# Performance work log

Measured on AMD Instinct MI355X. Metric: run time of the kernel, lower is better.

## Reference

```python
import jax, jax.numpy as jnp
import numpy as np

# Binary (sign) weight linear: y = x @ sign(W)^T + b

def _binarize(w):
    # sign with sign(0) mapped to +1, as in typical BinaryLinear impls
    return jnp.where(w >= 0, 1.0, -1.0).astype(w.dtype)

def setup_inputs() -> dict:
    key = jax.random.key(0)
    ks = jax.random.split(key, 7)
    B = 65536
    x = jax.random.normal(ks[0], (B, 28, 28), dtype=jnp.float32)
    W1 = jax.random.normal(ks[1], (1000, 784), dtype=jnp.float32) * 0.05
    b1 = jax.random.normal(ks[2], (1000,), dtype=jnp.float32) * 0.01
    W2 = jax.random.normal(ks[3], (500, 1000), dtype=jnp.float32) * 0.05
    b2 = jax.random.normal(ks[4], (500,), dtype=jnp.float32) * 0.01
    W3 = jax.random.normal(ks[5], (10, 500), dtype=jnp.float32) * 0.05
    b3 = jax.random.normal(ks[6], (10,), dtype=jnp.float32) * 0.01
    return {"x": x, "W1": W1, "b1": b1, "W2": W2, "b2": b2, "W3": W3, "b3": b3}

def reference(x, W1, b1, W2, b2, W3, b3):
    h = x.reshape(x.shape[0], -1)                      # [B, 784]
    h = jnp.maximum(h @ _binarize(W1).T + b1, 0.0)     # [B, 1000]
    h = jnp.maximum(h @ _binarize(W2).T + b2, 0.0)     # [B, 500]
    return h @ _binarize(W3).T + b3                    # [B, 10]
```

## Files before the change

kernel.cpp:

```cpp
#include <hip/hip_runtime.h>
#include <stdint.h>


typedef __attribute__((ext_vector_type(8))) short bf16x8;
typedef __attribute__((ext_vector_type(4))) float f32x4;

typedef const __attribute__((address_space(1))) unsigned int* as1_u32p;
typedef __attribute__((address_space(3))) unsigned int* as3_u32p;

__device__ __forceinline__ void glds16(const void* g, void* l) {
  __builtin_amdgcn_global_load_lds((as1_u32p)g, (as3_u32p)l, 16, 0, 0);
}

__device__ __forceinline__ unsigned short f2bf(float f) {
  union { float f; unsigned u; } c;
  c.f = f;
  unsigned u = c.u;
  u += 0x7FFFu + ((u >> 16) & 1u);
  return (unsigned short)(u >> 16);
}

__global__ void binarize_kernel(const float* __restrict__ src, int Ns, int Ks,
                                short* __restrict__ dst, int Np, int Kp) {
  int idx = blockIdx.x * 256 + threadIdx.x;
  if (idx >= Np * Kp) return;
  int n = idx / Kp;
  int k = idx - n * Kp;
  short v = 0;
  if (n < Ns && k < Ks)
    v = (src[n * Ks + k] >= 0.0f) ? (short)0x3F80 : (short)0xBF80;
  dst[idx] = v;
}

__global__ void convert_x_kernel(const float* __restrict__ X, short* __restrict__ Xp) {
  const int g = blockIdx.x * 256 + threadIdx.x;
  if (g >= 65536 * 104) return;
  const int row = g / 104;
  const int c = (g - row * 104) * 8;
  short tmp[8];
  if (c < 784) {
    const float* s = X + (size_t)row * 784 + c;
    float4 f0 = *(const float4*)s;
    float4 f1 = *(const float4*)(s + 4);
    tmp[0] = (short)f2bf(f0.x); tmp[1] = (short)f2bf(f0.y);
    tmp[2] = (short)f2bf(f0.z); tmp[3] = (short)f2bf(f0.w);
    tmp[4] = (short)f2bf(f1.x); tmp[5] = (short)f2bf(f1.y);
    tmp[6] = (short)f2bf(f1.z); tmp[7] = (short)f2bf(f1.w);
  } else {
#pragma unroll
    for (int i = 0; i < 8; ++i) tmp[i] = 0;
  }
  *(bf16x8*)(Xp + (size_t)row * 832 + c) = *(bf16x8*)(tmp);
}

template <int KP, int NKT, int NP, int NR, int NT>
__global__ __launch_bounds__(512, 2)
void gemm256(const short* __restrict__ A, const short* __restrict__ Wb,
             const float* __restrict__ bias, short* __restrict__ Hout) {
  __shared__ short Asm[2][256 * 64];
  __shared__ short Bsm[2][256 * 64];

  constexpr int NWG8 = (256 * NT) >> 3;
  const int d = blockIdx.x;
  const int lid = (d & 7) * NWG8 + (d >> 3);
  const int mi = lid / NT;
  const int ni = lid - mi * NT;
  const int m0 = mi << 8;
  const int n0 = ni << 8;
  const int start = (ni * NKT) / NT;

  const int tid = threadIdx.x;
  const int lane = tid & 63;
  const int w = tid >> 6;
  const int wm = w >> 2;
  const int wn = w & 3;
  const int l15 = lane & 15;
  const int quad = lane >> 4;

  const int srow = (w << 3) + (lane >> 3);
  const int scol = ((lane & 7) ^ (lane >> 3)) << 3;
  const short* ag = A + (size_t)(m0 + srow) * KP + scol;
  const short* bg = Wb + (size_t)(n0 + srow) * KP + scol;
  short* const la = &Asm[0][0] + (w << 9);
  short* const lb = &Bsm[0][0] + (w << 9);

  auto stageA = [&](int pb, int kit) {
    const short* s = ag + kit * 64;
    short* dst = la + (pb << 14);
    glds16(s, dst);
    glds16(s + (size_t)64 * KP, dst + 4096);
    glds16(s + (size_t)128 * KP, dst + 8192);
    glds16(s + (size_t)192 * KP, dst + 12288);
  };
  auto stageB = [&](int pb, int kit) {
    const short* s = bg + kit * 64;
    short* dst = lb + (pb << 14);
    glds16(s, dst);
    glds16(s + (size_t)64 * KP, dst + 4096);
    glds16(s + (size_t)128 * KP, dst + 8192);
    glds16(s + (size_t)192 * KP, dst + 12288);
  };

  const int arow = ((wm << 7) + l15) << 6;
  const int brow = ((wn << 6) + l15) << 6;
  const int sl0 = (quad ^ (lane & 7)) << 3;
  const int sl1 = sl0 ^ 32;

  f32x4 acc[8][4];
#pragma unroll
  for (int i = 0; i < 8; ++i)
#pragma unroll
    for (int j = 0; j < 4; ++j) acc[i][j] = (f32x4){0.f, 0.f, 0.f, 0.f};

  int k1 = start + 1; if (k1 >= NKT) k1 -= NKT;
  stageA(0, start); stageB(0, start);
  stageA(1, k1);    stageB(1, k1);
  asm volatile("s_waitcnt vmcnt(8)" ::: "memory");
  __builtin_amdgcn_s_barrier();

  for (int it = 0; it < NKT; ++it) {
    const int pb = it & 1;
    const short* Ab = &Asm[pb][0];
    const short* Bb = &Bsm[pb][0];

    bf16x8 a0[8], b0[4], a1[8], b1[4];
#pragma unroll
    for (int i = 0; i < 8; ++i) a0[i] = *(const bf16x8*)(Ab + arow + i * 1024 + sl0);
#pragma unroll
    for (int j = 0; j < 4; ++j) b0[j] = *(const bf16x8*)(Bb + brow + j * 1024 + sl0);
    __builtin_amdgcn_s_barrier();
    __builtin_amdgcn_s_setprio(1);
#pragma unroll
    for (int i = 0; i < 4; ++i)
#pragma unroll
      for (int j = 0; j < 4; ++j)
        acc[i][j] = __builtin_amdgcn_mfma_f32_16x16x32_bf16(a0[i], b0[j], acc[i][j], 0, 0, 0);
    __builtin_amdgcn_s_setprio(0);

    #pragma unroll
    for (int i = 0; i < 8; ++i) a1[i] = *(const bf16x8*)(Ab + arow + i * 1024 + sl1);
#pragma unroll
    for (int j = 0; j < 4; ++j) b1[j] = *(const bf16x8*)(Bb + brow + j * 1024 + sl1);
    __builtin_amdgcn_s_barrier();
    asm volatile("s_waitcnt lgkmcnt(0)" ::: "memory");
    __builtin_amdgcn_s_setprio(1);
#pragma unroll
    for (int i = 4; i < 8; ++i)
#pragma unroll
      for (int j = 0; j < 4; ++j)
        acc[i][j] = __builtin_amdgcn_mfma_f32_16x16x32_bf16(a0[i], b0[j], acc[i][j], 0, 0, 0);
    __builtin_amdgcn_s_setprio(0);
    __builtin_amdgcn_s_barrier();

    const int it2 = it + 2;
    int kit2 = start + it2; if (kit2 >= NKT) kit2 -= NKT;
    const bool stg = (it2 < NKT);
    if (stg) stageA(pb, kit2);
    __builtin_amdgcn_s_setprio(1);
#pragma unroll
    for (int i = 0; i < 4; ++i)
#pragma unroll
      for (int j = 0; j < 4; ++j)
        acc[i][j] = __builtin_amdgcn_mfma_f32_16x16x32_bf16(a1[i], b1[j], acc[i][j], 0, 0, 0);
    __builtin_amdgcn_s_setprio(0);
    if (stg) stageB(pb, kit2);
    __builtin_amdgcn_s_setprio(1);
#pragma unroll
    for (int i = 4; i < 8; ++i)
#pragma unroll
      for (int j = 0; j < 4; ++j)
        acc[i][j] = __builtin_amdgcn_mfma_f32_16x16x32_bf16(a1[i], b1[j], acc[i][j], 0, 0, 0);
    __builtin_amdgcn_s_setprio(0);
    if (stg) asm volatile("s_waitcnt vmcnt(8)" ::: "memory");
    else     asm volatile("s_waitcnt vmcnt(0)" ::: "memory");
    __builtin_amdgcn_s_barrier();
  }

#pragma unroll
  for (int j = 0; j < 4; ++j) {
    const int n = n0 + (wn << 6) + (j << 4) + l15;
    const float bv = (n < NR) ? bias[n] : 0.f;
#pragma unroll
    for (int i = 0; i < 8; ++i) {
      const int mr = m0 + (wm << 7) + (i << 4) + (quad << 2);
#pragma unroll
      for (int r = 0; r < 4; ++r) {
        float v = acc[i][j][r] + bv;
        v = v > 0.f ? v : 0.f;
        Hout[(size_t)(mr + r) * NP + n] = (short)f2bf(v);
      }
    }
  }
}

__global__ __launch_bounds__(256, 2)
void gemm1_fused_kernel(const float* __restrict__ X, const short* __restrict__ Wb,
                        const float* __restrict__ bias, short* __restrict__ H) {
  constexpr int K = 784, KP = 832, NP = 1024, NR = 1000;
  __shared__ short As[128 * 32];
  __shared__ short Bs[128 * 32];

  const int tid = threadIdx.x;
  const int lane = tid & 63;
  const int wave = tid >> 6;
  const int wm = wave >> 1, wn = wave & 1;
  const int l15 = lane & 15;
  const int quad = lane >> 4;
  const int m0 = blockIdx.y * 128;
  const int n0 = blockIdx.x * 128;

  const int ar = tid >> 1;
  const int aks = (tid & 1) * 16;
  const float* xrow = X + (size_t)(m0 + ar) * K;
  short* adst = As + ar * 32 + aks;

  const int br = wave * 16 + (lane >> 2);
  const int bks = (lane & 3) * 8;
  const short* brow0 = Wb + (size_t)(n0 + br) * KP + bks;
  short* bdst = Bs + (wave * 16) * 32;

  f32x4 acc[4][4];
#pragma unroll
  for (int i = 0; i < 4; ++i)
#pragma unroll
    for (int j2 = 0; j2 < 4; ++j2) acc[i][j2] = (f32x4){0.f, 0.f, 0.f, 0.f};

  for (int k0 = 0; k0 < KP; k0 += 32) {
    glds16(brow0 + k0, bdst);
    glds16(brow0 + k0 + (size_t)64 * KP, bdst + 64 * 32);
    short tmp[16];
#pragma unroll
    for (int c = 0; c < 4; ++c) {
      const int kk = k0 + aks + c * 4;
      float4 f;
      if (kk + 3 < K)
        f = *(const float4*)(xrow + kk);
      else
        f = make_float4(0.f, 0.f, 0.f, 0.f);
      tmp[c * 4 + 0] = (short)f2bf(f.x);
      tmp[c * 4 + 1] = (short)f2bf(f.y);
      tmp[c * 4 + 2] = (short)f2bf(f.z);
      tmp[c * 4 + 3] = (short)f2bf(f.w);
    }
    *(bf16x8*)(adst) = *(bf16x8*)(tmp);
    *(bf16x8*)(adst + 8) = *(bf16x8*)(tmp + 8);
    __syncthreads();

    const short* abase = As + (size_t)(wm * 64 + l15) * 32 + quad * 8;
    const short* bbase = Bs + (size_t)(wn * 64 + l15) * 32 + quad * 8;
    bf16x8 af[4], bfr[4];
#pragma unroll
    for (int i = 0; i < 4; ++i) af[i] = *(const bf16x8*)(abase + i * 16 * 32);
#pragma unroll
    for (int j2 = 0; j2 < 4; ++j2) bfr[j2] = *(const bf16x8*)(bbase + j2 * 16 * 32);
#pragma unroll
    for (int i = 0; i < 4; ++i)
#pragma unroll
      for (int j2 = 0; j2 < 4; ++j2)
        acc[i][j2] = __builtin_amdgcn_mfma_f32_16x16x32_bf16(af[i], bfr[j2], acc[i][j2], 0, 0, 0);
    __syncthreads();
  }

#pragma unroll
  for (int j2 = 0; j2 < 4; ++j2) {
    const int n = n0 + wn * 64 + j2 * 16 + l15;
    const float bv = (n < NR) ? bias[n] : 0.f;
#pragma unroll
    for (int i = 0; i < 4; ++i) {
      const int mr = m0 + wm * 64 + i * 16 + quad * 4;
#pragma unroll
      for (int r = 0; r < 4; ++r) {
        float v = acc[i][j2][r] + bv;
        v = v > 0.f ? v : 0.f;
        H[(size_t)(mr + r) * NP + n] = (short)f2bf(v);
      }
    }
  }
}

__global__ __launch_bounds__(256, 2)
void gemm3_kernel(const short* __restrict__ Hin, const short* __restrict__ Wb,
                  const float* __restrict__ bias, float* __restrict__ Out) {
  constexpr int KP = 512;
  __shared__ short As[64 * KP];

  const int tid = threadIdx.x;
  const int lane = tid & 63;
  const int wave = tid >> 6;
  const int l15 = lane & 15;
  const int quad = lane >> 4;
  const int m0 = blockIdx.x * 64;

  bf16x8 bw[16];
#pragma unroll
  for (int kk = 0; kk < 16; ++kk)
    bw[kk] = *(const bf16x8*)(Wb + l15 * KP + kk * 32 + quad * 8);

  const short* asrc = Hin + (size_t)(m0 + wave * 16) * KP + lane * 8;
  short* adst = As + (size_t)(wave * 16) * KP;
#pragma unroll
  for (int t = 0; t < 16; ++t)
    glds16(asrc + (size_t)t * KP, adst + (size_t)t * KP);

  __syncthreads();

  f32x4 acc = (f32x4){0.f, 0.f, 0.f, 0.f};
  const short* abase = As + (size_t)(wave * 16 + l15) * KP + quad * 8;
#pragma unroll
  for (int kk = 0; kk < 16; ++kk) {
    bf16x8 af = *(const bf16x8*)(abase + kk * 32);
    acc = __builtin_amdgcn_mfma_f32_16x16x32_bf16(af, bw[kk], acc, 0, 0, 0);
  }

  if (l15 < 10) {
    const float bv = bias[l15];
#pragma unroll
    for (int r = 0; r < 4; ++r) {
      const int mr = m0 + wave * 16 + quad * 4 + r;
      Out[(size_t)mr * 10 + l15] = acc[r] + bv;
    }
  }
}

extern "C" void kernel_launch(void* const* d_in, const int* in_sizes, int n_in,
                              void* d_out, int out_size, void* d_ws, size_t ws_size,
                              hipStream_t stream) {
  const float* x = (const float*)d_in[0];
  const float* W1 = (const float*)d_in[1];
  const float* b1 = (const float*)d_in[2];
  const float* W2 = (const float*)d_in[3];
  const float* b2 = (const float*)d_in[4];
  const float* W3 = (const float*)d_in[5];
  const float* b3 = (const float*)d_in[6];
  float* out = (float*)d_out;

  const size_t szW1 = (size_t)1024 * 832 * 2;
  const size_t szW2 = (size_t)512 * 1024 * 2;
  const size_t szW3 = (size_t)16 * 512 * 2;
  const size_t szH1 = (size_t)65536 * 1024 * 2;
  const size_t szXp = (size_t)65536 * 832 * 2;
  const size_t need = szW1 + szW2 + szW3 + szH1 + szXp;

  uint8_t* p = (uint8_t*)d_ws;
  short* W1b = (short*)p; p += szW1;
  short* W2b = (short*)p; p += szW2;
  short* W3b = (short*)p; p += szW3;
  short* h1 = (short*)p; p += szH1;
  short* Z = (short*)p;

  binarize_kernel<<<(1024 * 832 + 255) / 256, 256, 0, stream>>>(W1, 1000, 784, W1b, 1024, 832);
  binarize_kernel<<<(512 * 1024 + 255) / 256, 256, 0, stream>>>(W2, 500, 1000, W2b, 512, 1024);
  binarize_kernel<<<(16 * 512 + 255) / 256, 256, 0, stream>>>(W3, 10, 500, W3b, 16, 512);

  if (ws_size >= need) {
    short* Xp = Z;
    short* h2 = Z;
    convert_x_kernel<<<(65536 * 104 + 255) / 256, 256, 0, stream>>>(x, Xp);
    gemm256<832, 13, 1024, 1000, 4><<<1024, 512, 0, stream>>>(Xp, W1b, b1, h1);
    gemm256<1024, 16, 512, 500, 2><<<512, 512, 0, stream>>>(h1, W2b, b2, h2);
    gemm3_kernel<<<1024, 256, 0, stream>>>(h2, W3b, b3, out);
  } else {
    short* h2 = Z;
    gemm1_fused_kernel<<<dim3(8, 512), 256, 0, stream>>>(x, W1b, b1, h1);
    gemm256<1024, 16, 512, 500, 2><<<512, 512, 0, stream>>>(h1, W2b, b2, h2);
    gemm3_kernel<<<1024, 256, 0, stream>>>(h2, W3b, b3, out);
  }
}
```

Measured before the change: 581.4 us.

## Fuse fp32-to-bf16 input conversion into 256-tile GEMM1 and stage epilogue through LDS

```diff
diff --git a/kernel.cpp b/kernel.cpp
--- a/kernel.cpp
+++ b/kernel.cpp
@@ -32,33 +32,11 @@
   dst[idx] = v;
 }
 
-__global__ void convert_x_kernel(const float* __restrict__ X, short* __restrict__ Xp) {
-  const int g = blockIdx.x * 256 + threadIdx.x;
-  if (g >= 65536 * 104) return;
-  const int row = g / 104;
-  const int c = (g - row * 104) * 8;
-  short tmp[8];
-  if (c < 784) {
-    const float* s = X + (size_t)row * 784 + c;
-    float4 f0 = *(const float4*)s;
-    float4 f1 = *(const float4*)(s + 4);
-    tmp[0] = (short)f2bf(f0.x); tmp[1] = (short)f2bf(f0.y);
-    tmp[2] = (short)f2bf(f0.z); tmp[3] = (short)f2bf(f0.w);
-    tmp[4] = (short)f2bf(f1.x); tmp[5] = (short)f2bf(f1.y);
-    tmp[6] = (short)f2bf(f1.z); tmp[7] = (short)f2bf(f1.w);
-  } else {
-#pragma unroll
-    for (int i = 0; i < 8; ++i) tmp[i] = 0;
-  }
-  *(bf16x8*)(Xp + (size_t)row * 832 + c) = *(bf16x8*)(tmp);
-}
-
-template <int KP, int NKT, int NP, int NR, int NT>
 __global__ __launch_bounds__(512, 2)
-void gemm256(const short* __restrict__ A, const short* __restrict__ Wb,
-             const float* __restrict__ bias, short* __restrict__ Hout) {
-  __shared__ short Asm[2][256 * 64];
-  __shared__ short Bsm[2][256 * 64];
+void gemm1_fused256(const float* __restrict__ X, const short* __restrict__ Wb,
+                    const float* __restrict__ bias, short* __restrict__ Hout) {
+  constexpr int XK = 784, KPB = 832, NKT = 13, NP = 1024, NR = 1000, NT = 4;
+  __shared__ short LB[65536];
 
   constexpr int NWG8 = (256 * NT) >> 3;
   const int d = blockIdx.x;
@@ -79,10 +57,197 @@
 
   const int srow = (w << 3) + (lane >> 3);
   const int scol = ((lane & 7) ^ (lane >> 3)) << 3;
+  const short* bg = Wb + (size_t)(n0 + srow) * KPB + scol;
+  short* const lbW = LB + 32768 + (w << 9);
+  auto stageB = [&](int pb, int kit) {
+    const short* s = bg + kit * 64;
+    short* dst = lbW + (pb << 14);
+    glds16(s, dst);
+    glds16(s + (size_t)64 * KPB, dst + 4096);
+    glds16(s + (size_t)128 * KPB, dst + 8192);
+    glds16(s + (size_t)192 * KPB, dst + 12288);
+  };
+
+  const int arw = tid >> 1;
+  const float* xrow = X + (size_t)(m0 + arw) * XK;
+  float4 dA[4];
+  auto loadA = [&](int kit, int h) {
+    const int kb = kit * 64 + ((tid & 1) << 5) + (h << 4);
+#pragma unroll
+    for (int q = 0; q < 4; ++q) {
+      if (kb + q * 4 < XK)
+        dA[q] = *(const float4*)(xrow + kb + q * 4);
+      else
+        dA[q] = make_float4(0.f, 0.f, 0.f, 0.f);
+    }
+  };
+  auto cvtwrA = [&](int pb, int h) {
+    unsigned pk[8];
+#pragma unroll
+    for (int q = 0; q < 4; ++q) {
+      asm("v_cvt_pk_bf16_f32 %0, %1, %2" : "=v"(pk[2 * q]) : "v"(dA[q].x), "v"(dA[q].y));
+      asm("v_cvt_pk_bf16_f32 %0, %1, %2" : "=v"(pk[2 * q + 1]) : "v"(dA[q].z), "v"(dA[q].w));
+    }
+    short* ar = LB + (pb << 14) + (arw << 6);
+    const int c0 = ((tid & 1) << 2) + (h << 1);
+    *(uint4*)(ar + (((c0) ^ (arw & 7)) << 3)) = make_uint4(pk[0], pk[1], pk[2], pk[3]);
+    *(uint4*)(ar + (((c0 + 1) ^ (arw & 7)) << 3)) = make_uint4(pk[4], pk[5], pk[6], pk[7]);
+  };
+
+  const int arow = ((wm << 7) + l15) << 6;
+  const int brow = ((wn << 6) + l15) << 6;
+  const int sl0 = (quad ^ (lane & 7)) << 3;
+  const int sl1 = sl0 ^ 32;
+
+  f32x4 acc[8][4];
+#pragma unroll
+  for (int i = 0; i < 8; ++i)
+#pragma unroll
+    for (int j = 0; j < 4; ++j) acc[i][j] = (f32x4){0.f, 0.f, 0.f, 0.f};
+
+  int kt1 = start + 1; if (kt1 >= NKT) kt1 -= NKT;
+  loadA(start, 0);
+  asm volatile("s_waitcnt vmcnt(0)" ::: "memory");
+  cvtwrA(0, 0);
+  loadA(start, 1); stageB(0, start);
+  asm volatile("s_waitcnt vmcnt(4)" ::: "memory");
+  cvtwrA(0, 1);
+  loadA(kt1, 0); stageB(1, kt1);
+  asm volatile("s_waitcnt vmcnt(4)" ::: "memory");
+  cvtwrA(1, 0);
+  loadA(kt1, 1);
+  asm volatile("s_waitcnt vmcnt(0)" ::: "memory");
+  cvtwrA(1, 1);
+  asm volatile("s_waitcnt lgkmcnt(0)" ::: "memory");
+  __builtin_amdgcn_s_barrier();
+
+  for (int it = 0; it < NKT; ++it) {
+    const int pb = it & 1;
+    const short* Ab = LB + (pb << 14);
+    const short* Bb = LB + 32768 + (pb << 14);
+    int kit2 = start + it + 2; if (kit2 >= NKT) kit2 -= NKT;
+    const bool stg = (it + 2 < NKT);
+
+    bf16x8 a0[8], b0[4], a1[8], b1[4];
+#pragma unroll
+    for (int i = 0; i < 8; ++i) a0[i] = *(const bf16x8*)(Ab + arow + i * 1024 + sl0);
+#pragma unroll
+    for (int j = 0; j < 4; ++j) b0[j] = *(const bf16x8*)(Bb + brow + j * 1024 + sl0);
+    if (stg) loadA(kit2, 0);
+    __builtin_amdgcn_s_setprio(1);
+#pragma unroll
+    for (int i = 0; i < 4; ++i)
+#pragma unroll
+      for (int j = 0; j < 4; ++j)
+        acc[i][j] = __builtin_amdgcn_mfma_f32_16x16x32_bf16(a0[i], b0[j], acc[i][j], 0, 0, 0);
+    __builtin_amdgcn_s_setprio(0);
+
+#pragma unroll
+    for (int i = 0; i < 8; ++i) a1[i] = *(const bf16x8*)(Ab + arow + i * 1024 + sl1);
+#pragma unroll
+    for (int j = 0; j < 4; ++j) b1[j] = *(const bf16x8*)(Bb + brow + j * 1024 + sl1);
+    __builtin_amdgcn_s_setprio(1);
+#pragma unroll
+    for (int i = 4; i < 8; ++i)
+#pragma unroll
+      for (int j = 0; j < 4; ++j)
+        acc[i][j] = __builtin_amdgcn_mfma_f32_16x16x32_bf16(a0[i], b0[j], acc[i][j], 0, 0, 0);
+    __builtin_amdgcn_s_setprio(0);
+    asm volatile("s_waitcnt lgkmcnt(0)" ::: "memory");
+    __builtin_amdgcn_s_barrier();
+
+    asm volatile("s_waitcnt vmcnt(0)" ::: "memory");
+    if (stg) {
+      cvtwrA(pb, 0);
+      loadA(kit2, 1);
+    }
+    __builtin_amdgcn_s_setprio(1);
+#pragma unroll
+    for (int i = 0; i < 4; ++i)
+#pragma unroll
+      for (int j = 0; j < 4; ++j)
+        acc[i][j] = __builtin_amdgcn_mfma_f32_16x16x32_bf16(a1[i], b1[j], acc[i][j], 0, 0, 0);
+    __builtin_amdgcn_s_setprio(0);
+
+    if (stg) {
+      asm volatile("s_waitcnt vmcnt(0)" ::: "memory");
+      cvtwrA(pb, 1);
+      stageB(pb, kit2);
+    }
+    __builtin_amdgcn_s_setprio(1);
+#pragma unroll
+    for (int i = 4; i < 8; ++i)
+#pragma unroll
+      for (int j = 0; j < 4; ++j)
+        acc[i][j] = __builtin_amdgcn_mfma_f32_16x16x32_bf16(a1[i], b1[j], acc[i][j], 0, 0, 0);
+    __builtin_amdgcn_s_setprio(0);
+    asm volatile("s_waitcnt lgkmcnt(0)" ::: "memory");
+    __builtin_amdgcn_s_barrier();
+  }
+
+  short* C = LB;
+#pragma unroll
+  for (int j = 0; j < 4; ++j) {
+    const int col = (wn << 6) + (j << 4) + l15;
+    const int n = n0 + col;
+    const float bv = (n < NR) ? bias[n] : 0.f;
+#pragma unroll
+    for (int i = 0; i < 8; ++i) {
+      const int row0 = (wm << 7) + (i << 4) + (quad << 2);
+#pragma unroll
+      for (int r = 0; r < 4; ++r) {
+        float v = acc[i][j][r] + bv;
+        v = v > 0.f ? v : 0.f;
+        const int row = row0 + r;
+        const int sw = ((((col >> 3) ^ (row & 7))) << 3) | (col & 7);
+        C[(row << 8) + sw] = (short)f2bf(v);
+      }
+    }
+  }
+  __syncthreads();
+  {
+    const int row = tid >> 1;
+    const int ch = (tid & 1) << 4;
+    short* gout = Hout + (size_t)(m0 + row) * NP + n0;
+#pragma unroll
+    for (int v2 = 0; v2 < 16; ++v2) {
+      const int c = ch + v2;
+      const int sc = c ^ (row & 7);
+      bf16x8 dv = *(const bf16x8*)(C + (row << 8) + (sc << 3));
+      *(bf16x8*)(gout + (c << 3)) = dv;
+    }
+  }
+}
+
+template <int KP, int NKT, int NP, int NR, int NT>
+__global__ __launch_bounds__(512, 2)
+void gemm256(const short* __restrict__ A, const short* __restrict__ Wb,
+             const float* __restrict__ bias, short* __restrict__ Hout) {
+  __shared__ short LB[65536];
+
+  constexpr int NWG8 = (256 * NT) >> 3;
+  const int d = blockIdx.x;
+  const int lid = (d & 7) * NWG8 + (d >> 3);
+  const int mi = lid / NT;
+  const int ni = lid - mi * NT;
+  const int m0 = mi << 8;
+  const int n0 = ni << 8;
+  const int start = (ni * NKT) / NT;
+
+  const int tid = threadIdx.x;
+  const int lane = tid & 63;
+  const int w = tid >> 6;
+  const int wm = w >> 2;
+  const int wn = w & 3;
+  const int l15 = lane & 15;
+  const int quad = lane >> 4;
+
+  const int srow = (w << 3) + (lane >> 3);
+  const int scol = ((lane & 7) ^ (lane >> 3)) << 3;
   const short* ag = A + (size_t)(m0 + srow) * KP + scol;
   const short* bg = Wb + (size_t)(n0 + srow) * KP + scol;
-  short* const la = &Asm[0][0] + (w << 9);
-  short* const lb = &Bsm[0][0] + (w << 9);
+  short* const la = LB + (w << 9);
+  short* const lb = LB + 32768 + (w << 9);
 
   auto stageA = [&](int pb, int kit) {
     const short* s = ag + kit * 64;
@@ -112,57 +277,55 @@
 #pragma unroll
     for (int j = 0; j < 4; ++j) acc[i][j] = (f32x4){0.f, 0.f, 0.f, 0.f};
 
-  int k1 = start + 1; if (k1 >= NKT) k1 -= NKT;
+  int kt1 = start + 1; if (kt1 >= NKT) kt1 -= NKT;
   stageA(0, start); stageB(0, start);
-  stageA(1, k1);    stageB(1, k1);
+  stageA(1, kt1);   stageB(1, kt1);
   asm volatile("s_waitcnt vmcnt(8)" ::: "memory");
   __builtin_amdgcn_s_barrier();
 
   for (int it = 0; it < NKT; ++it) {
     const int pb = it & 1;
-    const short* Ab = &Asm[pb][0];
-    const short* Bb = &Bsm[pb][0];
+    const short* Ab = LB + (pb << 14);
+    const short* Bb = LB + 32768 + (pb << 14);
+    int kit2 = start + it + 2; if (kit2 >= NKT) kit2 -= NKT;
+    const bool stg = (it + 2 < NKT);
 
     bf16x8 a0[8], b0[4], a1[8], b1[4];
 #pragma unroll
     for (int i = 0; i < 8; ++i) a0[i] = *(const bf16x8*)(Ab + arow + i * 1024 + sl0);
 #pragma unroll
     for (int j = 0; j < 4; ++j) b0[j] = *(const bf16x8*)(Bb + brow + j * 1024 + sl0);
+    __builtin_amdgcn_s_setprio(1);
+#pragma unroll
+    for (int i = 0; i < 4; ++i)
+#pragma unroll
+      for (int j = 0; j < 4; ++j)
+        acc[i][j] = __builtin_amdgcn_mfma_f32_16x16x32_bf16(a0[i], b0[j], acc[i][j], 0, 0, 0);
+    __builtin_amdgcn_s_setprio(0);
+
+#pragma unroll
+    for (int i = 0; i < 8; ++i) a1[i] = *(const bf16x8*)(Ab + arow + i * 1024 + sl1);
+#pragma unroll
+    for (int j = 0; j < 4; ++j) b1[j] = *(const bf16x8*)(Bb + brow + j * 1024 + sl1);
+    __builtin_amdgcn_s_setprio(1);
+#pragma unroll
+    for (int i = 4; i < 8; ++i)
+#pragma unroll
+      for (int j = 0; j < 4; ++j)
+        acc[i][j] = __builtin_amdgcn_mfma_f32_16x16x32_bf16(a0[i], b0[j], acc[i][j], 0, 0, 0);
+    __builtin_amdgcn_s_setprio(0);
+    asm volatile("s_waitcnt lgkmcnt(0)" ::: "memory");
     __builtin_amdgcn_s_barrier();
+
+    if (stg) stageA(pb, kit2);
     __builtin_amdgcn_s_setprio(1);
 #pragma unroll
     for (int i = 0; i < 4; ++i)
 #pragma unroll
       for (int j = 0; j < 4; ++j)
-        acc[i][j] = __builtin_amdgcn_mfma_f32_16x16x32_bf16(a0[i], b0[j], acc[i][j], 0, 0, 0);
-    __builtin_amdgcn_s_setprio(0);
-
-    #pragma unroll
-    for (int i = 0; i < 8; ++i) a1[i] = *(const bf16x8*)(Ab + arow + i * 1024 + sl1);
-#pragma unroll
-    for (int j = 0; j < 4; ++j) b1[j] = *(const bf16x8*)(Bb + brow + j * 1024 + sl1);
-    __builtin_amdgcn_s_barrier();
-    asm volatile("s_waitcnt lgkmcnt(0)" ::: "memory");
-    __builtin_amdgcn_s_setprio(1);
-#pragma unroll
-    for (int i = 4; i < 8; ++i)
-#pragma unroll
-      for (int j = 0; j < 4; ++j)
-        acc[i][j] = __builtin_amdgcn_mfma_f32_16x16x32_bf16(a0[i], b0[j], acc[i][j], 0, 0, 0);
-    __builtin_amdgcn_s_setprio(0);
-    __builtin_amdgcn_s_barrier();
-
-    const int it2 = it + 2;
-    int kit2 = start + it2; if (kit2 >= NKT) kit2 -= NKT;
-    const bool stg = (it2 < NKT);
-    if (stg) stageA(pb, kit2);
-    __builtin_amdgcn_s_setprio(1);
-#pragma unroll
-    for (int i = 0; i < 4; ++i)
-#pragma unroll
-      for (int j = 0; j < 4; ++j)
         acc[i][j] = __builtin_amdgcn_mfma_f32_16x16x32_bf16(a1[i], b1[j], acc[i][j], 0, 0, 0);
     __builtin_amdgcn_s_setprio(0);
+
     if (stg) stageB(pb, kit2);
     __builtin_amdgcn_s_setprio(1);
 #pragma unroll
@@ -176,104 +339,36 @@
     __builtin_amdgcn_s_barrier();
   }
 
+  short* C = LB;
 #pragma unroll
   for (int j = 0; j < 4; ++j) {
-    const int n = n0 + (wn << 6) + (j << 4) + l15;
+    const int col = (wn << 6) + (j << 4) + l15;
+    const int n = n0 + col;
     const float bv = (n < NR) ? bias[n] : 0.f;
 #pragma unroll
     for (int i = 0; i < 8; ++i) {
-      const int mr = m0 + (wm << 7) + (i << 4) + (quad << 2);
+      const int row0 = (wm << 7) + (i << 4) + (quad << 2);
 #pragma unroll
       for (int r = 0; r < 4; ++r) {
         float v = acc[i][j][r] + bv;
         v = v > 0.f ? v : 0.f;
-        Hout[(size_t)(mr + r) * NP + n] = (short)f2bf(v);
+        const int row = row0 + r;
+        const int sw = ((((col >> 3) ^ (row & 7))) << 3) | (col & 7);
+        C[(row << 8) + sw] = (short)f2bf(v);
       }
     }
   }
-}
-
-__global__ __launch_bounds__(256, 2)
-void gemm1_fused_kernel(const float* __restrict__ X, const short* __restrict__ Wb,
-                        const float* __restrict__ bias, short* __restrict__ H) {
-  constexpr int K = 784, KP = 832, NP = 1024, NR = 1000;
-  __shared__ short As[128 * 32];
-  __shared__ short Bs[128 * 32];
-
-  const int tid = threadIdx.x;
-  const int lane = tid & 63;
-  const int wave = tid >> 6;
-  const int wm = wave >> 1, wn = wave & 1;
-  const int l15 = lane & 15;
-  const int quad = lane >> 4;
-  const int m0 = blockIdx.y * 128;
-  const int n0 = blockIdx.x * 128;
-
-  const int ar = tid >> 1;
-  const int aks = (tid & 1) * 16;
-  const float* xrow = X + (size_t)(m0 + ar) * K;
-  short* adst = As + ar * 32 + aks;
-
-  const int br = wave * 16 + (lane >> 2);
-  const int bks = (lane & 3) * 8;
-  const short* brow0 = Wb + (size_t)(n0 + br) * KP + bks;
-  short* bdst = Bs + (wave * 16) * 32;
-
-  f32x4 acc[4][4];
-#pragma unroll
-  for (int i = 0; i < 4; ++i)
-#pragma unroll
-    for (int j2 = 0; j2 < 4; ++j2) acc[i][j2] = (f32x4){0.f, 0.f, 0.f, 0.f};
-
-  for (int k0 = 0; k0 < KP; k0 += 32) {
-    glds16(brow0 + k0, bdst);
-    glds16(brow0 + k0 + (size_t)64 * KP, bdst + 64 * 32);
-    short tmp[16];
-#pragma unroll
-    for (int c = 0; c < 4; ++c) {
-      const int kk = k0 + aks + c * 4;
-      float4 f;
-      if (kk + 3 < K)
-        f = *(const float4*)(xrow + kk);
-      else
-        f = make_float4(0.f, 0.f, 0.f, 0.f);
-      tmp[c * 4 + 0] = (short)f2bf(f.x);
-      tmp[c * 4 + 1] = (short)f2bf(f.y);
-      tmp[c * 4 + 2] = (short)f2bf(f.z);
-      tmp[c * 4 + 3] = (short)f2bf(f.w);
-    }
-    *(bf16x8*)(adst) = *(bf16x8*)(tmp);
-    *(bf16x8*)(adst + 8) = *(bf16x8*)(tmp + 8);
-    __syncthreads();
-
-    const short* abase = As + (size_t)(wm * 64 + l15) * 32 + quad * 8;
-    const short* bbase = Bs + (size_t)(wn * 64 + l15) * 32 + quad * 8;
-    bf16x8 af[4], bfr[4];
-#pragma unroll
-    for (int i = 0; i < 4; ++i) af[i] = *(const bf16x8*)(abase + i * 16 * 32);
-#pragma unroll
-    for (int j2 = 0; j2 < 4; ++j2) bfr[j2] = *(const bf16x8*)(bbase + j2 * 16 * 32);
-#pragma unroll
-    for (int i = 0; i < 4; ++i)
-#pragma unroll
-      for (int j2 = 0; j2 < 4; ++j2)
-        acc[i][j2] = __builtin_amdgcn_mfma_f32_16x16x32_bf16(af[i], bfr[j2], acc[i][j2], 0, 0, 0);
-    __syncthreads();
-  }
-
-#pragma unroll
-  for (int j2 = 0; j2 < 4; ++j2) {
-    const int n = n0 + wn * 64 + j2 * 16 + l15;
-    const float bv = (n < NR) ? bias[n] : 0.f;
-#pragma unroll
-    for (int i = 0; i < 4; ++i) {
-      const int mr = m0 + wm * 64 + i * 16 + quad * 4;
-#pragma unroll
-      for (int r = 0; r < 4; ++r) {
-        float v = acc[i][j2][r] + bv;
-        v = v > 0.f ? v : 0.f;
-        H[(size_t)(mr + r) * NP + n] = (short)f2bf(v);
-      }
+  __syncthreads();
+  {
+    const int row = tid >> 1;
+    const int ch = (tid & 1) << 4;
+    short* gout = Hout + (size_t)(m0 + row) * NP + n0;
+#pragma unroll
+    for (int v2 = 0; v2 < 16; ++v2) {
+      const int c = ch + v2;
+      const int sc = c ^ (row & 7);
+      bf16x8 dv = *(const bf16x8*)(C + (row << 8) + (sc << 3));
+      *(bf16x8*)(gout + (c << 3)) = dv;
     }
   }
 }
@@ -338,31 +433,19 @@
   const size_t szW2 = (size_t)512 * 1024 * 2;
   const size_t szW3 = (size_t)16 * 512 * 2;
   const size_t szH1 = (size_t)65536 * 1024 * 2;
-  const size_t szXp = (size_t)65536 * 832 * 2;
-  const size_t need = szW1 + szW2 + szW3 + szH1 + szXp;
 
   uint8_t* p = (uint8_t*)d_ws;
   short* W1b = (short*)p; p += szW1;
   short* W2b = (short*)p; p += szW2;
   short* W3b = (short*)p; p += szW3;
   short* h1 = (short*)p; p += szH1;
-  short* Z = (short*)p;
+  short* h2 = (short*)p;
 
   binarize_kernel<<<(1024 * 832 + 255) / 256, 256, 0, stream>>>(W1, 1000, 784, W1b, 1024, 832);
   binarize_kernel<<<(512 * 1024 + 255) / 256, 256, 0, stream>>>(W2, 500, 1000, W2b, 512, 1024);
   binarize_kernel<<<(16 * 512 + 255) / 256, 256, 0, stream>>>(W3, 10, 500, W3b, 16, 512);
 
-  if (ws_size >= need) {
-    short* Xp = Z;
-    short* h2 = Z;
-    convert_x_kernel<<<(65536 * 104 + 255) / 256, 256, 0, stream>>>(x, Xp);
-    gemm256<832, 13, 1024, 1000, 4><<<1024, 512, 0, stream>>>(Xp, W1b, b1, h1);
-    gemm256<1024, 16, 512, 500, 2><<<512, 512, 0, stream>>>(h1, W2b, b2, h2);
-    gemm3_kernel<<<1024, 256, 0, stream>>>(h2, W3b, b3, out);
-  } else {
-    short* h2 = Z;
-    gemm1_fused_kernel<<<dim3(8, 512), 256, 0, stream>>>(x, W1b, b1, h1);
-    gemm256<1024, 16, 512, 500, 2><<<512, 512, 0, stream>>>(h1, W2b, b2, h2);
-    gemm3_kernel<<<1024, 256, 0, stream>>>(h2, W3b, b3, out);
-  }
-}
+  gemm1_fused256<<<1024, 512, 0, stream>>>(x, W1b, b1, h1);
+  gemm256<1024, 16, 512, 500, 2><<<512, 512, 0, stream>>>(h1, W2b, b2, h2);
+  gemm3_kernel<<<1024, 256, 0, stream>>>(h2, W3b, b3, out);
+}
```

Measured after the change: 672.0 us. 15.6% more time.

## Replace 256x256 GEMM tile with 128x256 tile and BK=32 pipeline

Applied to the files above, without the earlier changes.

```diff
diff --git a/kernel.cpp b/kernel.cpp
--- a/kernel.cpp
+++ b/kernel.cpp
@@ -54,18 +54,18 @@
 }
 
 template <int KP, int NKT, int NP, int NR, int NT>
-__global__ __launch_bounds__(512, 2)
-void gemm256(const short* __restrict__ A, const short* __restrict__ Wb,
-             const float* __restrict__ bias, short* __restrict__ Hout) {
-  __shared__ short Asm[2][256 * 64];
-  __shared__ short Bsm[2][256 * 64];
-
-  constexpr int NWG8 = (256 * NT) >> 3;
+__global__ __launch_bounds__(512, 4)
+void gemm128x256(const short* __restrict__ A, const short* __restrict__ Wb,
+                 const float* __restrict__ bias, short* __restrict__ Hout) {
+  __shared__ short Abuf[2][128 * 32];
+  __shared__ short Bbuf[2][256 * 32];
+
+  constexpr int NWG8 = (512 * NT) >> 3;
   const int d = blockIdx.x;
   const int lid = (d & 7) * NWG8 + (d >> 3);
   const int mi = lid / NT;
   const int ni = lid - mi * NT;
-  const int m0 = mi << 8;
+  const int m0 = mi << 7;
   const int n0 = ni << 8;
   const int start = (ni * NKT) / NT;
 
@@ -77,117 +77,91 @@
   const int l15 = lane & 15;
   const int quad = lane >> 4;
 
-  const int srow = (w << 3) + (lane >> 3);
-  const int scol = ((lane & 7) ^ (lane >> 3)) << 3;
-  const short* ag = A + (size_t)(m0 + srow) * KP + scol;
-  const short* bg = Wb + (size_t)(n0 + srow) * KP + scol;
-  short* const la = &Asm[0][0] + (w << 9);
-  short* const lb = &Bsm[0][0] + (w << 9);
+  const int srow = tid >> 2;
+  const int sslot = tid & 3;
+  const int gcol = ((sslot ^ ((srow >> 1) & 3)) << 3);
+  const short* ag = A + (size_t)(m0 + srow) * KP + gcol;
+  const short* bg = Wb + (size_t)(n0 + srow) * KP + gcol;
+  const int ldsw = w << 9;
 
   auto stageA = [&](int pb, int kit) {
-    const short* s = ag + kit * 64;
-    short* dst = la + (pb << 14);
-    glds16(s, dst);
-    glds16(s + (size_t)64 * KP, dst + 4096);
-    glds16(s + (size_t)128 * KP, dst + 8192);
-    glds16(s + (size_t)192 * KP, dst + 12288);
+    glds16(ag + kit * 32, &Abuf[pb][ldsw]);
   };
   auto stageB = [&](int pb, int kit) {
-    const short* s = bg + kit * 64;
-    short* dst = lb + (pb << 14);
-    glds16(s, dst);
-    glds16(s + (size_t)64 * KP, dst + 4096);
-    glds16(s + (size_t)128 * KP, dst + 8192);
-    glds16(s + (size_t)192 * KP, dst + 12288);
+    const short* s = bg + kit * 32;
+    glds16(s, &Bbuf[pb][ldsw]);
+    glds16(s + (size_t)128 * KP, &Bbuf[pb][ldsw + 4096]);
   };
 
-  const int arow = ((wm << 7) + l15) << 6;
-  const int brow = ((wn << 6) + l15) << 6;
-  const int sl0 = (quad ^ (lane & 7)) << 3;
-  const int sl1 = sl0 ^ 32;
-
-  f32x4 acc[8][4];
-#pragma unroll
-  for (int i = 0; i < 8; ++i)
+  const int sl = (quad ^ ((l15 >> 1) & 3)) << 3;
+  const int abase = ((wm << 6) + l15) * 32 + sl;
+  const int bbase = ((wn << 6) + l15) * 32 + sl;
+
+  f32x4 acc[4][4];
+#pragma unroll
+  for (int i = 0; i < 4; ++i)
 #pragma unroll
     for (int j = 0; j < 4; ++j) acc[i][j] = (f32x4){0.f, 0.f, 0.f, 0.f};
 
-  int k1 = start + 1; if (k1 >= NKT) k1 -= NKT;
+  int kt1 = start + 1; if (kt1 >= NKT) kt1 -= NKT;
   stageA(0, start); stageB(0, start);
-  stageA(1, k1);    stageB(1, k1);
-  asm volatile("s_waitcnt vmcnt(8)" ::: "memory");
+  stageA(1, kt1);   stageB(1, kt1);
+  asm volatile("s_waitcnt vmcnt(3)" ::: "memory");
   __builtin_amdgcn_s_barrier();
 
   for (int it = 0; it < NKT; ++it) {
     const int pb = it & 1;
-    const short* Ab = &Asm[pb][0];
-    const short* Bb = &Bsm[pb][0];
-
-    bf16x8 a0[8], b0[4], a1[8], b1[4];
-#pragma unroll
-    for (int i = 0; i < 8; ++i) a0[i] = *(const bf16x8*)(Ab + arow + i * 1024 + sl0);
-#pragma unroll
-    for (int j = 0; j < 4; ++j) b0[j] = *(const bf16x8*)(Bb + brow + j * 1024 + sl0);
+    const short* Ab = &Abuf[pb][0];
+    const short* Bb = &Bbuf[pb][0];
+    int kit2 = start + it + 2; if (kit2 >= NKT) kit2 -= NKT;
+    const bool stg = (it + 2 < NKT);
+
+    bf16x8 af[4], bf[4];
+#pragma unroll
+    for (int i = 0; i < 4; ++i) af[i] = *(const bf16x8*)(Ab + abase + i * 512);
+#pragma unroll
+    for (int j = 0; j < 4; ++j) bf[j] = *(const bf16x8*)(Bb + bbase + j * 512);
+
+    __builtin_amdgcn_s_setprio(1);
+#pragma unroll
+    for (int i = 0; i < 2; ++i)
+#pragma unroll
+      for (int j = 0; j < 4; ++j)
+        acc[i][j] = __builtin_amdgcn_mfma_f32_16x16x32_bf16(af[i], bf[j], acc[i][j], 0, 0, 0);
+    __builtin_amdgcn_s_setprio(0);
+    asm volatile("s_waitcnt lgkmcnt(0)" ::: "memory");
     __builtin_amdgcn_s_barrier();
+
+    if (stg) { stageA(pb, kit2); stageB(pb, kit2); }
     __builtin_amdgcn_s_setprio(1);
 #pragma unroll
-    for (int i = 0; i < 4; ++i)
+    for (int i = 2; i < 4; ++i)
 #pragma unroll
       for (int j = 0; j < 4; ++j)
-        acc[i][j] = __builtin_amdgcn_mfma_f32_16x16x32_bf16(a0[i], b0[j], acc[i][j], 0, 0, 0);
+        acc[i][j] = __builtin_amdgcn_mfma_f32_16x16x32_bf16(af[i], bf[j], acc[i][j], 0, 0, 0);
     __builtin_amdgcn_s_setprio(0);
-
-    #pragma unroll
-    for (int i = 0; i < 8; ++i) a1[i] = *(const bf16x8*)(Ab + arow + i * 1024 + sl1);
-#pragma unroll
-    for (int j = 0; j < 4; ++j) b1[j] = *(const bf16x8*)(Bb + brow + j * 1024 + sl1);
-    __builtin_amdgcn_s_barrier();
-    asm volatile("s_waitcnt lgkmcnt(0)" ::: "memory");
-    __builtin_amdgcn_s_setprio(1);
-#pragma unroll
-    for (int i = 4; i < 8; ++i)
-#pragma unroll
-      for (int j = 0; j < 4; ++j)
-        acc[i][j] = __builtin_amdgcn_mfma_f32_16x16x32_bf16(a0[i], b0[j], acc[i][j], 0, 0, 0);
-    __builtin_amdgcn_s_setprio(0);
-    __builtin_amdgcn_s_barrier();
-
-    const int it2 = it + 2;
-    int kit2 = start + it2; if (kit2 >= NKT) kit2 -= NKT;
-    const bool stg = (it2 < NKT);
-    if (stg) stageA(pb, kit2);
-    __builtin_amdgcn_s_setprio(1);
-#pragma unroll
-    for (int i = 0; i < 4; ++i)
-#pragma unroll
-      for (int j = 0; j < 4; ++j)
-        acc[i][j] = __builtin_amdgcn_mfma_f32_16x16x32_bf16(a1[i], b1[j], acc[i][j], 0, 0, 0);
-    __builtin_amdgcn_s_setprio(0);
-    if (stg) stageB(pb, kit2);
-    __builtin_amdgcn_s_setprio(1);
-#pragma unroll
-    for (int i = 4; i < 8; ++i)
-#pragma unroll
-      for (int j = 0; j < 4; ++j)
-        acc[i][j] = __builtin_amdgcn_mfma_f32_16x16x32_bf16(a1[i], b1[j], acc[i][j], 0, 0, 0);
-    __builtin_amdgcn_s_setprio(0);
-    if (stg) asm volatile("s_waitcnt vmcnt(8)" ::: "memory");
+    if (stg) asm volatile("s_waitcnt vmcnt(3)" ::: "memory");
     else     asm volatile("s_waitcnt vmcnt(0)" ::: "memory");
     __builtin_amdgcn_s_barrier();
   }
 
+  float bv[4];
 #pragma unroll
   for (int j = 0; j < 4; ++j) {
     const int n = n0 + (wn << 6) + (j << 4) + l15;
-    const float bv = (n < NR) ? bias[n] : 0.f;
-#pragma unroll
-    for (int i = 0; i < 8; ++i) {
-      const int mr = m0 + (wm << 7) + (i << 4) + (quad << 2);
-#pragma unroll
-      for (int r = 0; r < 4; ++r) {
-        float v = acc[i][j][r] + bv;
+    bv[j] = (n < NR) ? bias[n] : 0.f;
+  }
+#pragma unroll
+  for (int i = 0; i < 4; ++i) {
+#pragma unroll
+    for (int r = 0; r < 4; ++r) {
+      const int mr = m0 + (wm << 6) + (i << 4) + (quad << 2) + r;
+      short* rowp = Hout + (size_t)mr * NP + n0 + (wn << 6) + l15;
+#pragma unroll
+      for (int j = 0; j < 4; ++j) {
+        float v = acc[i][j][r] + bv[j];
         v = v > 0.f ? v : 0.f;
-        Hout[(size_t)(mr + r) * NP + n] = (short)f2bf(v);
+        rowp[j << 4] = (short)f2bf(v);
       }
     }
   }
@@ -356,13 +330,13 @@
     short* Xp = Z;
     short* h2 = Z;
     convert_x_kernel<<<(65536 * 104 + 255) / 256, 256, 0, stream>>>(x, Xp);
-    gemm256<832, 13, 1024, 1000, 4><<<1024, 512, 0, stream>>>(Xp, W1b, b1, h1);
-    gemm256<1024, 16, 512, 500, 2><<<512, 512, 0, stream>>>(h1, W2b, b2, h2);
+    gemm128x256<832, 26, 1024, 1000, 4><<<2048, 512, 0, stream>>>(Xp, W1b, b1, h1);
+    gemm128x256<1024, 32, 512, 500, 2><<<1024, 512, 0, stream>>>(h1, W2b, b2, h2);
     gemm3_kernel<<<1024, 256, 0, stream>>>(h2, W3b, b3, out);
   } else {
     short* h2 = Z;
     gemm1_fused_kernel<<<dim3(8, 512), 256, 0, stream>>>(x, W1b, b1, h1);
-    gemm256<1024, 16, 512, 500, 2><<<512, 512, 0, stream>>>(h1, W2b, b2, h2);
+    gemm128x256<1024, 32, 512, 500, 2><<<1024, 512, 0, stream>>>(h1, W2b, b2, h2);
     gemm3_kernel<<<1024, 256, 0, stream>>>(h2, W3b, b3, out);
   }
 }
```

Result: faster. 530.1 us (-8.8%).
